# Optimization experiments

Hardware: AMD Instinct MI355X
Metric: run time of the kernel (lower is better)

The kernel has to match this reference:

```python
import jax, jax.numpy as jnp
import numpy as np
from jax import lax

EMBED_DIM = 384
NUM_GROUPS = 128
GROUP_SIZE = 64
LN_EPS = 1e-5


def setup_inputs() -> dict:
    key = jax.random.key(0)
    k_pts, k1, k2, k3, k4 = jax.random.split(key, 5)
    B, N = 32, 16384
    points = jax.random.normal(k_pts, (B, N, 3), dtype=jnp.float32)
    # local_mlp: Linear(3,128) -> GELU -> Linear(128, embed_dim)
    w1 = jax.random.normal(k1, (3, 128), dtype=jnp.float32) * (1.0 / np.sqrt(3))
    b1 = jax.random.normal(k2, (128,), dtype=jnp.float32) * 0.01
    w2 = jax.random.normal(k3, (128, EMBED_DIM), dtype=jnp.float32) * (1.0 / np.sqrt(128))
    b2 = jax.random.normal(k4, (EMBED_DIM,), dtype=jnp.float32) * 0.01
    ln_scale = jnp.ones((EMBED_DIM,), dtype=jnp.float32)
    ln_bias = jnp.zeros((EMBED_DIM,), dtype=jnp.float32)
    return {"points": points, "w1": w1, "b1": b1, "w2": w2, "b2": b2,
            "ln_scale": ln_scale, "ln_bias": ln_bias}


def _farthest_point_sample(points, num_samples):
    # points: [B, N, 3]. Deterministic start at index 0 (torch uses randint).
    B, N, _ = points.shape

    def step(carry, _):
        distance, farthest = carry  # [B, N], [B]
        centroid = jnp.take_along_axis(points, farthest[:, None, None], axis=1)  # [B,1,3]
        d = jnp.sum((points - centroid) ** 2, axis=-1)  # [B, N]
        distance = jnp.minimum(distance, d)
        nxt = jnp.argmax(distance, axis=-1).astype(jnp.int32)
        return (distance, nxt), farthest

    init = (jnp.full((B, N), jnp.inf, dtype=points.dtype),
            jnp.zeros((B,), dtype=jnp.int32))
    _, idx = lax.scan(step, init, None, length=num_samples)  # [S, B]
    return idx.T  # [B, S]


def reference(points, w1, b1, w2, b2, ln_scale, ln_bias):
    B, N, _ = points.shape
    centroid_idx = _farthest_point_sample(points, NUM_GROUPS)  # [B, G]
    centroids = jnp.take_along_axis(
        points, centroid_idx[:, :, None].astype(jnp.int32), axis=1)  # [B, G, 3]

    # squared distances (same ordering as torch.cdist for topk); matmul form
    # avoids materializing a [B, G, N, 3] diff tensor.
    c2 = jnp.sum(centroids ** 2, axis=-1)  # [B, G]
    p2 = jnp.sum(points ** 2, axis=-1)     # [B, N]
    dist2 = c2[:, :, None] + p2[:, None, :] - 2.0 * jnp.einsum(
        'bgc,bnc->bgn', centroids, points)  # [B, G, N]

    # k smallest -> top_k of negated distances
    _, neighbor_idx = lax.top_k(-dist2, GROUP_SIZE)  # [B, G, K]

    batch_ix = jnp.arange(B)[:, None, None]
    grouped = points[batch_ix, neighbor_idx]  # [B, G, K, 3]
    local_coords = grouped - centroids[:, :, None, :]  # [B, G, K, 3]

    h = jax.nn.gelu(local_coords @ w1 + b1, approximate=False)  # [B,G,K,128]
    feats = h @ w2 + b2  # [B, G, K, D]
    tokens = jnp.mean(feats, axis=2)  # [B, G, D]

    mu = jnp.mean(tokens, axis=-1, keepdims=True)
    var = jnp.mean((tokens - mu) ** 2, axis=-1, keepdims=True)
    tokens_ln = (tokens - mu) * lax.rsqrt(var + LN_EPS) * ln_scale + ln_bias
    return centroids, tokens_ln
```

## Files before the change

### kernel.cpp

```cpp
#include <hip/hip_runtime.h>
#include <math.h>

#define BB 32
#define NN 16384
#define GG 128
#define KK 64
#define HH 128
#define DD 384
#define LN_EPS 1e-5f
#define CAP 1024

__device__ __forceinline__ float sq3(float x, float y, float z) {
    return __fadd_rn(__fadd_rn(__fmul_rn(x, x), __fmul_rn(y, y)), __fmul_rn(z, z));
}

__device__ __forceinline__ unsigned distkey(float px, float py, float pz, float4 c4) {
    float p2 = sq3(px, py, pz);
    float dot = __fadd_rn(__fadd_rn(__fmul_rn(c4.x, px), __fmul_rn(c4.y, py)),
                          __fmul_rn(c4.z, pz));
    float d = __fsub_rn(__fadd_rn(c4.w, p2), __fmul_rn(2.0f, dot));
    unsigned u = __float_as_uint(d);
    return u ^ ((u & 0x80000000u) ? 0xFFFFFFFFu : 0x80000000u);
}

__device__ __forceinline__ unsigned lanerank(unsigned long long m) {
    unsigned r = __builtin_amdgcn_mbcnt_lo((unsigned)m, 0);
    return __builtin_amdgcn_mbcnt_hi((unsigned)(m >> 32), r);
}

__global__ void prep_kernel(const float* __restrict__ w2, float* __restrict__ w2t) {
    int i = blockIdx.x * 256 + threadIdx.x;
    if (i < HH * DD) {
        int f = i >> 7, k = i & 127;
        w2t[i] = w2[k * DD + f];
    }
}

__global__ __launch_bounds__(1024, 4) void fps_kernel(const float* __restrict__ pts,
                                                      float* __restrict__ cent_out,
                                                      float4* __restrict__ cent_pad) {
    __shared__ float4 ds4[NN / 4];
    __shared__ unsigned long long slot[GG];
    const int b = blockIdx.x;
    const int tid = threadIdx.x;
    const float* p = pts + (size_t)b * NN * 3;
    const float4* p4 = (const float4*)p;

    for (int i = tid; i < NN / 4; i += 1024)
        ds4[i] = make_float4(INFINITY, INFINITY, INFINITY, INFINITY);
    for (int i = tid; i < GG; i += 1024) slot[i] = 0ull;
    __syncthreads();

    float cx = p[0], cy = p[1], cz = p[2];

    for (int it = 0; it < GG; it++) {
        if (tid == 0) {
            float* co = cent_out + ((size_t)b * GG + it) * 3;
            co[0] = cx; co[1] = cy; co[2] = cz;
            cent_pad[b * GG + it] = make_float4(cx, cy, cz, sq3(cx, cy, cz));
        }
        if (it == GG - 1) break;

        float bv0 = -INFINITY, bv1 = -INFINITY, bv2 = -INFINITY, bv3 = -INFINITY;
        int bq0 = 0, bq1 = 0, bq2 = 0, bq3 = 0;
#pragma unroll
        for (int j = 0; j < 4; j++) {
            int q = tid + j * 1024;
            float4 A = p4[3 * q], B = p4[3 * q + 1], C = p4[3 * q + 2];
            float4 dv = ds4[q];
            float d0 = sq3(__fsub_rn(A.x, cx), __fsub_rn(A.y, cy), __fsub_rn(A.z, cz));
            float d1 = sq3(__fsub_rn(A.w, cx), __fsub_rn(B.x, cy), __fsub_rn(B.y, cz));
            float d2 = sq3(__fsub_rn(B.z, cx), __fsub_rn(B.w, cy), __fsub_rn(C.x, cz));
            float d3 = sq3(__fsub_rn(C.y, cx), __fsub_rn(C.z, cy), __fsub_rn(C.w, cz));
            float n0 = fminf(dv.x, d0), n1 = fminf(dv.y, d1);
            float n2 = fminf(dv.z, d2), n3 = fminf(dv.w, d3);
            bool ch = (d0 < dv.x) | (d1 < dv.y) | (d2 < dv.z) | (d3 < dv.w);
            if (ch) ds4[q] = make_float4(n0, n1, n2, n3);
            if (n0 > bv0) { bv0 = n0; bq0 = q; }
            if (n1 > bv1) { bv1 = n1; bq1 = q; }
            if (n2 > bv2) { bv2 = n2; bq2 = q; }
            if (n3 > bv3) { bv3 = n3; bq3 = q; }
        }
        float fv = bv0; int fi = 4 * bq0;
        {
            int i1 = 4 * bq1 + 1, i2 = 4 * bq2 + 2, i3 = 4 * bq3 + 3;
            if (bv1 > fv || (bv1 == fv && i1 < fi)) { fv = bv1; fi = i1; }
            if (bv2 > fv || (bv2 == fv && i2 < fi)) { fv = bv2; fi = i2; }
            if (bv3 > fv || (bv3 == fv && i3 < fi)) { fv = bv3; fi = i3; }
        }
#pragma unroll
        for (int off = 32; off >= 1; off >>= 1) {
            float ov = __shfl_down(fv, off);
            int oi = __shfl_down(fi, off);
            if (ov > fv || (ov == fv && oi < fi)) { fv = ov; fi = oi; }
        }
        if ((tid & 63) == 0) {
            unsigned long long packed =
                ((unsigned long long)__float_as_uint(fv) << 32) |
                (unsigned)(0xFFFFFFFFu - (unsigned)fi);
            atomicMax(&slot[it], packed);
        }
        __syncthreads();
        unsigned long long w = slot[it];
        int idx = (int)(0xFFFFFFFFu - (unsigned)w);
        const float* wp = p + (size_t)idx * 3;
        cx = wp[0]; cy = wp[1]; cz = wp[2];
    }
}

__global__ __launch_bounds__(256, 4) void group_kernel(
    const float* __restrict__ pts, const float4* __restrict__ cent_pad,
    const float* __restrict__ w1, const float* __restrict__ b1,
    const float* __restrict__ w2t, const float* __restrict__ b2,
    const float* __restrict__ lns, const float* __restrict__ lnb,
    float* __restrict__ tok_out) {
    __shared__ unsigned candKey[4][CAP];
    __shared__ unsigned short candIdx[4][CAP];
    __shared__ unsigned short tieIdx[4][128];
    __shared__ unsigned short selIdx[4][KK];
    __shared__ float4 localPt[4][KK];
    __shared__ __align__(16) float hbar[4][HH];

    const int tid = threadIdx.x, lane = tid & 63, wid = tid >> 6;
    const int x = blockIdx.x & 7, j = blockIdx.x >> 3;
    const int b = x * 4 + (j >> 5);
    const int g = ((j & 31) << 2) + wid;
    const float* p = pts + (size_t)b * NN * 3;
    const float4* p4 = (const float4*)p;
    float4 c4 = cent_pad[b * GG + g];

    unsigned sk[8];
#pragma unroll
    for (int s = 0; s < 8; s++) {
        int n = (s * 64 + lane) * 32;
        sk[s] = distkey(p[n * 3], p[n * 3 + 1], p[n * 3 + 2], c4);
    }
    auto sample_kth = [&](int rank) -> unsigned {
        unsigned T = 0u;
        for (int bit = 31; bit >= 0; bit--) {
            unsigned c = T | (1u << bit);
            int cnt = 0;
#pragma unroll
            for (int s = 0; s < 8; s++) cnt += __popcll(__ballot(sk[s] < c));
            if (cnt < rank) T = c;
        }
        return T;
    };
    unsigned* ck = candKey[wid];
    unsigned short* ci = candIdx[wid];

    unsigned T1 = sample_kth(16);
    int cnt;
    {
        int base = 0;
        for (int u = 0; u < 32; u++) {
            int qa = u * 128 + lane, qb = qa + 64;
            float4 Aa = p4[3 * qa], Ba = p4[3 * qa + 1], Ca = p4[3 * qa + 2];
            float4 Ab = p4[3 * qb], Bb2 = p4[3 * qb + 1], Cb = p4[3 * qb + 2];
#pragma unroll
            for (int t = 0; t < 2; t++) {
                int q = t ? qb : qa;
                float4 A = t ? Ab : Aa, Bv = t ? Bb2 : Ba, Cv = t ? Cb : Ca;
                unsigned kk[4];
                kk[0] = distkey(A.x, A.y, A.z, c4);
                kk[1] = distkey(A.w, Bv.x, Bv.y, c4);
                kk[2] = distkey(Bv.z, Bv.w, Cv.x, c4);
                kk[3] = distkey(Cv.y, Cv.z, Cv.w, c4);
#pragma unroll
                for (int qq = 0; qq < 4; qq++) {
                    bool pred = kk[qq] <= T1;
                    unsigned long long m = __ballot(pred);
                    if (pred) {
                        int pos = base + (int)lanerank(m);
                        if (pos < CAP) {
                            ck[pos] = kk[qq];
                            ci[pos] = (unsigned short)(4 * q + qq);
                        }
                    }
                    base += __popcll(m);
                }
            }
            if ((u & 3) == 3) __syncthreads();
        }
        cnt = base;
    }

    auto collect_ns = [&](unsigned T) -> int {
        int base = 0;
        for (int it2 = 0; it2 < 64; it2++) {
            int q = it2 * 64 + lane;
            float4 A = p4[3 * q], Bv = p4[3 * q + 1], Cv = p4[3 * q + 2];
            unsigned kk[4];
            kk[0] = distkey(A.x, A.y, A.z, c4);
            kk[1] = distkey(A.w, Bv.x, Bv.y, c4);
            kk[2] = distkey(Bv.z, Bv.w, Cv.x, c4);
            kk[3] = distkey(Cv.y, Cv.z, Cv.w, c4);
#pragma unroll
            for (int qq = 0; qq < 4; qq++) {
                bool pred = kk[qq] <= T;
                unsigned long long m = __ballot(pred);
                if (pred) {
                    int pos = base + (int)lanerank(m);
                    if (pos < CAP) {
                        ck[pos] = kk[qq];
                        ci[pos] = (unsigned short)(4 * q + qq);
                    }
                }
                base += __popcll(m);
            }
        }
        return base;
    };
    if (cnt > CAP) cnt = collect_ns(sample_kth(8));

    bool fallback = (cnt < KK || cnt > CAP);
    if (!fallback) {
        unsigned k8[16];
#pragma unroll
        for (int r = 0; r < 16; r++) {
            int s = r * 64 + lane;
            k8[r] = (s < cnt) ? ck[s] : 0xFFFFFFFFu;
        }
        unsigned T = 0u;
        for (int bit = 31; bit >= 0; bit--) {
            unsigned c = T | (1u << bit);
            int cl = 0;
#pragma unroll
            for (int r = 0; r < 16; r++) cl += __popcll(__ballot(k8[r] < c));
            if (cl < KK) T = c;
        }
        int cless = 0;
#pragma unroll
        for (int r = 0; r < 16; r++) cless += __popcll(__ballot(k8[r] < T));
        int need = KK - cless;
        int base2 = 0;
#pragma unroll
        for (int r = 0; r < 16; r++) {
            bool pr = k8[r] < T;
            unsigned long long m = __ballot(pr);
            if (pr) selIdx[wid][base2 + lanerank(m)] = ci[r * 64 + lane];
            base2 += __popcll(m);
        }
        int tb = 0;
#pragma unroll
        for (int r = 0; r < 16; r++) {
            bool pr = (r * 64 + lane < cnt) && (k8[r] == T);
            unsigned long long m = __ballot(pr);
            if (pr) {
                int pos = tb + (int)lanerank(m);
                if (pos < 128) tieIdx[wid][pos] = ci[r * 64 + lane];
            }
            tb += __popcll(m);
        }
        if (tb > 128) {
            fallback = true;
        } else {
#pragma unroll
            for (int rr = 0; rr < 2; rr++) {
                int t = lane + rr * 64;
                if (t < tb) {
                    unsigned short my = tieIdx[wid][t];
                    int rank = 0;
                    for (int j2 = 0; j2 < tb; j2++) rank += (tieIdx[wid][j2] < my);
                    if (rank < need) selIdx[wid][cless + rank] = my;
                }
            }
        }
    }
    if (fallback) {
        unsigned long long last = 0ull;
        for (int r = 0; r < KK; r++) {
            unsigned long long best = ~0ull;
            for (int it2 = 0; it2 < 64; it2++) {
                int q = it2 * 64 + lane;
                float4 A = p4[3 * q], Bv = p4[3 * q + 1], Cv = p4[3 * q + 2];
                unsigned kk[4];
                kk[0] = distkey(A.x, A.y, A.z, c4);
                kk[1] = distkey(A.w, Bv.x, Bv.y, c4);
                kk[2] = distkey(Bv.z, Bv.w, Cv.x, c4);
                kk[3] = distkey(Cv.y, Cv.z, Cv.w, c4);
#pragma unroll
                for (int qq = 0; qq < 4; qq++) {
                    unsigned long long pp =
                        (((unsigned long long)kk[qq]) << 16) | (unsigned)(4 * q + qq);
                    if ((r == 0 || pp > last) && pp < best) best = pp;
                }
            }
#pragma unroll
            for (int off = 32; off >= 1; off >>= 1) {
                unsigned long long o = __shfl_xor(best, off);
                if (o < best) best = o;
            }
            selIdx[wid][r] = (unsigned short)(best & 0xFFFFu);
            last = best;
        }
    }
    __syncthreads();

    {
        int n = selIdx[wid][lane];
        localPt[wid][lane] =
            make_float4(p[n * 3] - c4.x, p[n * 3 + 1] - c4.y, p[n * 3 + 2] - c4.z, 0.f);
    }
    {
        float wa0 = w1[lane], wb0 = w1[HH + lane], wc0 = w1[2 * HH + lane], bb0 = b1[lane];
        float wa1 = w1[64 + lane], wb1 = w1[HH + 64 + lane], wc1 = w1[2 * HH + 64 + lane],
              bb1 = b1[64 + lane];
        float s0 = 0.f, s1 = 0.f;
        for (int k = 0; k < KK; k++) {
            float4 lp = localPt[wid][k];
            float a0 = lp.x * wa0 + lp.y * wb0 + lp.z * wc0 + bb0;
            float a1 = lp.x * wa1 + lp.y * wb1 + lp.z * wc1 + bb1;
            s0 += 0.5f * a0 * (1.0f + erff(a0 * 0.70710678118654752440f));
            s1 += 0.5f * a1 * (1.0f + erff(a1 * 0.70710678118654752440f));
        }
        hbar[wid][lane] = s0 * (1.0f / 64.0f);
        hbar[wid][64 + lane] = s1 * (1.0f / 64.0f);
    }
    {
        const int f0 = lane * 6;
        float acc0 = b2[f0], acc1 = b2[f0 + 1], acc2 = b2[f0 + 2];
        float acc3 = b2[f0 + 3], acc4 = b2[f0 + 4], acc5 = b2[f0 + 5];
        const float4* hb = (const float4*)hbar[wid];
        for (int q = 0; q < HH / 4; q++) {
            float4 h4 = hb[q];
            const float* w0 = w2t + (size_t)f0 * HH + 4 * q;
            float4 a = *(const float4*)(w0);
            float4 bq = *(const float4*)(w0 + HH);
            float4 cq = *(const float4*)(w0 + 2 * HH);
            float4 dq = *(const float4*)(w0 + 3 * HH);
            float4 eq = *(const float4*)(w0 + 4 * HH);
            float4 fq = *(const float4*)(w0 + 5 * HH);
            acc0 += h4.x * a.x + h4.y * a.y + h4.z * a.z + h4.w * a.w;
            acc1 += h4.x * bq.x + h4.y * bq.y + h4.z * bq.z + h4.w * bq.w;
            acc2 += h4.x * cq.x + h4.y * cq.y + h4.z * cq.z + h4.w * cq.w;
            acc3 += h4.x * dq.x + h4.y * dq.y + h4.z * dq.z + h4.w * dq.w;
            acc4 += h4.x * eq.x + h4.y * eq.y + h4.z * eq.z + h4.w * eq.w;
            acc5 += h4.x * fq.x + h4.y * fq.y + h4.z * fq.z + h4.w * fq.w;
        }
        float s1v = acc0 + acc1 + acc2 + acc3 + acc4 + acc5;
        float s2v = acc0 * acc0 + acc1 * acc1 + acc2 * acc2 + acc3 * acc3 +
                    acc4 * acc4 + acc5 * acc5;
#pragma unroll
        for (int off = 32; off >= 1; off >>= 1) {
            s1v += __shfl_xor(s1v, off);
            s2v += __shfl_xor(s2v, off);
        }
        float mu = s1v / (float)DD;
        float var = s2v / (float)DD - mu * mu;
        float rstd = rsqrtf(var + LN_EPS);
        float* outp = tok_out + ((size_t)b * GG + g) * DD + f0;
        outp[0] = (acc0 - mu) * rstd * lns[f0] + lnb[f0];
        outp[1] = (acc1 - mu) * rstd * lns[f0 + 1] + lnb[f0 + 1];
        outp[2] = (acc2 - mu) * rstd * lns[f0 + 2] + lnb[f0 + 2];
        outp[3] = (acc3 - mu) * rstd * lns[f0 + 3] + lnb[f0 + 3];
        outp[4] = (acc4 - mu) * rstd * lns[f0 + 4] + lnb[f0 + 4];
        outp[5] = (acc5 - mu) * rstd * lns[f0 + 5] + lnb[f0 + 5];
    }
}

extern "C" void kernel_launch(void* const* d_in, const int* in_sizes, int n_in,
                              void* d_out, int out_size, void* d_ws, size_t ws_size,
                              hipStream_t stream) {
    const float* pts = (const float*)d_in[0];
    const float* w1 = (const float*)d_in[1];
    const float* b1 = (const float*)d_in[2];
    const float* w2 = (const float*)d_in[3];
    const float* b2 = (const float*)d_in[4];
    const float* lns = (const float*)d_in[5];
    const float* lnb = (const float*)d_in[6];
    float* out = (float*)d_out;

    float4* cent_pad = (float4*)d_ws;
    float* w2t = (float*)((char*)d_ws + 65536);

    prep_kernel<<<192, 256, 0, stream>>>(w2, w2t);
    fps_kernel<<<BB, 1024, 0, stream>>>(pts, out, cent_pad);
    group_kernel<<<1024, 256, 0, stream>>>(pts, cent_pad, w1, b1, w2t, b2, lns, lnb,
                                           out + BB * GG * 3);
}
```

Baseline: 591.3 us.

## Fuse FPS and grouping into one persistent kernel with per-centroid ready flags

Merges the farthest-point-sampling kernel and the grouping/MLP kernel into one persistent kernel. The first 32 blocks run FPS and publish each centroid index through a global flag. Every wave, including FPS waves once they finish, pulls (batch, group) tasks from an atomic counter and spins until that centroid is ready. The goal is to overlap kNN and MLP work with the serial FPS iterations instead of waiting for FPS to complete. The candidate capacity shrinks and the sampled threshold rank changes to cut shared memory, at the cost of spin-waiting, a smaller CU footprint for FPS blocks, and more reliance on the fallback path.

```diff
diff --git a/kernel.cpp b/kernel.cpp
--- a/kernel.cpp
+++ b/kernel.cpp
@@ -8,7 +8,8 @@
 #define HH 128
 #define DD 384
 #define LN_EPS 1e-5f
-#define CAP 1024
+#define CAP 640
+#define NTASK (BB * GG)
 
 __device__ __forceinline__ float sq3(float x, float y, float z) {
     return __fadd_rn(__fadd_rn(__fmul_rn(x, x), __fmul_rn(y, y)), __fmul_rn(z, z));
@@ -28,139 +29,159 @@
     return __builtin_amdgcn_mbcnt_hi((unsigned)(m >> 32), r);
 }
 
-__global__ void prep_kernel(const float* __restrict__ w2, float* __restrict__ w2t) {
+__global__ void prep_kernel(const float* __restrict__ w2, float* __restrict__ w2t,
+                            unsigned* __restrict__ syncArea) {
     int i = blockIdx.x * 256 + threadIdx.x;
     if (i < HH * DD) {
         int f = i >> 7, k = i & 127;
         w2t[i] = w2[k * DD + f];
     }
-}
-
-__global__ __launch_bounds__(1024, 4) void fps_kernel(const float* __restrict__ pts,
-                                                      float* __restrict__ cent_out,
-                                                      float4* __restrict__ cent_pad) {
-    __shared__ float4 ds4[NN / 4];
+    if (i < NTASK + 64) syncArea[i] = 0u;
+}
+
+struct GrpSh {
+    unsigned candKey[16][CAP];
+    unsigned short candIdx[16][CAP];
+    unsigned short tieIdx[16][128];
+    unsigned short selIdx[16][KK];
+    float4 localPt[16][KK];
+    float hbar[16][HH];
+};
+struct FpsSh {
+    float4 ds4[NN / 4];
+};
+union ShU {
+    FpsSh f;
+    GrpSh g;
+};
+
+__global__ __launch_bounds__(1024) void fused_kernel(
+    const float* __restrict__ pts, const float* __restrict__ w1,
+    const float* __restrict__ b1, const float* __restrict__ w2t,
+    const float* __restrict__ b2, const float* __restrict__ lns,
+    const float* __restrict__ lnb, float* __restrict__ cent_out,
+    float* __restrict__ tok_out, unsigned* __restrict__ done,
+    unsigned* __restrict__ taskCtr) {
+    __shared__ ShU sh;
     __shared__ unsigned long long slot[GG];
-    const int b = blockIdx.x;
-    const int tid = threadIdx.x;
-    const float* p = pts + (size_t)b * NN * 3;
-    const float4* p4 = (const float4*)p;
-
-    for (int i = tid; i < NN / 4; i += 1024)
-        ds4[i] = make_float4(INFINITY, INFINITY, INFINITY, INFINITY);
-    for (int i = tid; i < GG; i += 1024) slot[i] = 0ull;
+    const int tid = threadIdx.x, lane = tid & 63, wid = tid >> 6;
+
+    if (blockIdx.x < BB) {
+        const int b = blockIdx.x;
+        const float* p = pts + (size_t)b * NN * 3;
+        const float4* p4 = (const float4*)p;
+        for (int i = tid; i < NN / 4; i += 1024)
+            sh.f.ds4[i] = make_float4(INFINITY, INFINITY, INFINITY, INFINITY);
+        for (int i = tid; i < GG; i += 1024) slot[i] = 0ull;
+        __syncthreads();
+
+        float cx = p[0], cy = p[1], cz = p[2];
+        int curIdx = 0;
+        for (int it = 0; it < GG; it++) {
+            if (tid == 0) {
+                float* co = cent_out + ((size_t)b * GG + it) * 3;
+                co[0] = cx; co[1] = cy; co[2] = cz;
+                __hip_atomic_store(&done[b * GG + it], (unsigned)(curIdx + 1),
+                                   __ATOMIC_RELAXED, __HIP_MEMORY_SCOPE_AGENT);
+            }
+            if (it == GG - 1) break;
+
+            float bv0 = -INFINITY, bv1 = -INFINITY, bv2 = -INFINITY, bv3 = -INFINITY;
+            int bq0 = 0, bq1 = 0, bq2 = 0, bq3 = 0;
+#pragma unroll
+            for (int j = 0; j < 4; j++) {
+                int q = tid + j * 1024;
+                float4 A = p4[3 * q], B = p4[3 * q + 1], C = p4[3 * q + 2];
+                float4 dv = sh.f.ds4[q];
+                float d0 = sq3(__fsub_rn(A.x, cx), __fsub_rn(A.y, cy), __fsub_rn(A.z, cz));
+                float d1 = sq3(__fsub_rn(A.w, cx), __fsub_rn(B.x, cy), __fsub_rn(B.y, cz));
+                float d2 = sq3(__fsub_rn(B.z, cx), __fsub_rn(B.w, cy), __fsub_rn(C.x, cz));
+                float d3 = sq3(__fsub_rn(C.y, cx), __fsub_rn(C.z, cy), __fsub_rn(C.w, cz));
+                float n0 = fminf(dv.x, d0), n1 = fminf(dv.y, d1);
+                float n2 = fminf(dv.z, d2), n3 = fminf(dv.w, d3);
+                bool ch = (d0 < dv.x) | (d1 < dv.y) | (d2 < dv.z) | (d3 < dv.w);
+                if (ch) sh.f.ds4[q] = make_float4(n0, n1, n2, n3);
+                if (n0 > bv0) { bv0 = n0; bq0 = q; }
+                if (n1 > bv1) { bv1 = n1; bq1 = q; }
+                if (n2 > bv2) { bv2 = n2; bq2 = q; }
+                if (n3 > bv3) { bv3 = n3; bq3 = q; }
+            }
+            float fv = bv0; int fi = 4 * bq0;
+            {
+                int i1 = 4 * bq1 + 1, i2 = 4 * bq2 + 2, i3 = 4 * bq3 + 3;
+                if (bv1 > fv || (bv1 == fv && i1 < fi)) { fv = bv1; fi = i1; }
+                if (bv2 > fv || (bv2 == fv && i2 < fi)) { fv = bv2; fi = i2; }
+                if (bv3 > fv || (bv3 == fv && i3 < fi)) { fv = bv3; fi = i3; }
+            }
+#pragma unroll
+            for (int off = 32; off >= 1; off >>= 1) {
+                float ov = __shfl_down(fv, off);
+                int oi = __shfl_down(fi, off);
+                if (ov > fv || (ov == fv && oi < fi)) { fv = ov; fi = oi; }
+            }
+            if ((tid & 63) == 0) {
+                unsigned long long packed =
+                    ((unsigned long long)__float_as_uint(fv) << 32) |
+                    (unsigned)(0xFFFFFFFFu - (unsigned)fi);
+                atomicMax(&slot[it], packed);
+            }
+            __syncthreads();
+            unsigned long long w = slot[it];
+            curIdx = (int)(0xFFFFFFFFu - (unsigned)w);
+            const float* wp = p + (size_t)curIdx * 3;
+            cx = wp[0]; cy = wp[1]; cz = wp[2];
+        }
+    }
     __syncthreads();
 
-    float cx = p[0], cy = p[1], cz = p[2];
-
-    for (int it = 0; it < GG; it++) {
-        if (tid == 0) {
-            float* co = cent_out + ((size_t)b * GG + it) * 3;
-            co[0] = cx; co[1] = cy; co[2] = cz;
-            cent_pad[b * GG + it] = make_float4(cx, cy, cz, sq3(cx, cy, cz));
-        }
-        if (it == GG - 1) break;
-
-        float bv0 = -INFINITY, bv1 = -INFINITY, bv2 = -INFINITY, bv3 = -INFINITY;
-        int bq0 = 0, bq1 = 0, bq2 = 0, bq3 = 0;
-#pragma unroll
-        for (int j = 0; j < 4; j++) {
-            int q = tid + j * 1024;
-            float4 A = p4[3 * q], B = p4[3 * q + 1], C = p4[3 * q + 2];
-            float4 dv = ds4[q];
-            float d0 = sq3(__fsub_rn(A.x, cx), __fsub_rn(A.y, cy), __fsub_rn(A.z, cz));
-            float d1 = sq3(__fsub_rn(A.w, cx), __fsub_rn(B.x, cy), __fsub_rn(B.y, cz));
-            float d2 = sq3(__fsub_rn(B.z, cx), __fsub_rn(B.w, cy), __fsub_rn(C.x, cz));
-            float d3 = sq3(__fsub_rn(C.y, cx), __fsub_rn(C.z, cy), __fsub_rn(C.w, cz));
-            float n0 = fminf(dv.x, d0), n1 = fminf(dv.y, d1);
-            float n2 = fminf(dv.z, d2), n3 = fminf(dv.w, d3);
-            bool ch = (d0 < dv.x) | (d1 < dv.y) | (d2 < dv.z) | (d3 < dv.w);
-            if (ch) ds4[q] = make_float4(n0, n1, n2, n3);
-            if (n0 > bv0) { bv0 = n0; bq0 = q; }
-            if (n1 > bv1) { bv1 = n1; bq1 = q; }
-            if (n2 > bv2) { bv2 = n2; bq2 = q; }
-            if (n3 > bv3) { bv3 = n3; bq3 = q; }
-        }
-        float fv = bv0; int fi = 4 * bq0;
-        {
-            int i1 = 4 * bq1 + 1, i2 = 4 * bq2 + 2, i3 = 4 * bq3 + 3;
-            if (bv1 > fv || (bv1 == fv && i1 < fi)) { fv = bv1; fi = i1; }
-            if (bv2 > fv || (bv2 == fv && i2 < fi)) { fv = bv2; fi = i2; }
-            if (bv3 > fv || (bv3 == fv && i3 < fi)) { fv = bv3; fi = i3; }
-        }
-#pragma unroll
-        for (int off = 32; off >= 1; off >>= 1) {
-            float ov = __shfl_down(fv, off);
-            int oi = __shfl_down(fi, off);
-            if (ov > fv || (ov == fv && oi < fi)) { fv = ov; fi = oi; }
-        }
-        if ((tid & 63) == 0) {
-            unsigned long long packed =
-                ((unsigned long long)__float_as_uint(fv) << 32) |
-                (unsigned)(0xFFFFFFFFu - (unsigned)fi);
-            atomicMax(&slot[it], packed);
-        }
-        __syncthreads();
-        unsigned long long w = slot[it];
-        int idx = (int)(0xFFFFFFFFu - (unsigned)w);
-        const float* wp = p + (size_t)idx * 3;
-        cx = wp[0]; cy = wp[1]; cz = wp[2];
-    }
-}
-
-__global__ __launch_bounds__(256, 4) void group_kernel(
-    const float* __restrict__ pts, const float4* __restrict__ cent_pad,
-    const float* __restrict__ w1, const float* __restrict__ b1,
-    const float* __restrict__ w2t, const float* __restrict__ b2,
-    const float* __restrict__ lns, const float* __restrict__ lnb,
-    float* __restrict__ tok_out) {
-    __shared__ unsigned candKey[4][CAP];
-    __shared__ unsigned short candIdx[4][CAP];
-    __shared__ unsigned short tieIdx[4][128];
-    __shared__ unsigned short selIdx[4][KK];
-    __shared__ float4 localPt[4][KK];
-    __shared__ __align__(16) float hbar[4][HH];
-
-    const int tid = threadIdx.x, lane = tid & 63, wid = tid >> 6;
-    const int x = blockIdx.x & 7, j = blockIdx.x >> 3;
-    const int b = x * 4 + (j >> 5);
-    const int g = ((j & 31) << 2) + wid;
-    const float* p = pts + (size_t)b * NN * 3;
-    const float4* p4 = (const float4*)p;
-    float4 c4 = cent_pad[b * GG + g];
-
-    unsigned sk[8];
-#pragma unroll
-    for (int s = 0; s < 8; s++) {
-        int n = (s * 64 + lane) * 32;
-        sk[s] = distkey(p[n * 3], p[n * 3 + 1], p[n * 3 + 2], c4);
-    }
-    auto sample_kth = [&](int rank) -> unsigned {
-        unsigned T = 0u;
-        for (int bit = 31; bit >= 0; bit--) {
-            unsigned c = T | (1u << bit);
-            int cnt = 0;
-#pragma unroll
-            for (int s = 0; s < 8; s++) cnt += __popcll(__ballot(sk[s] < c));
-            if (cnt < rank) T = c;
-        }
-        return T;
-    };
-    unsigned* ck = candKey[wid];
-    unsigned short* ci = candIdx[wid];
-
-    unsigned T1 = sample_kth(16);
-    int cnt;
-    {
-        int base = 0;
-        for (int u = 0; u < 32; u++) {
-            int qa = u * 128 + lane, qb = qa + 64;
-            float4 Aa = p4[3 * qa], Ba = p4[3 * qa + 1], Ca = p4[3 * qa + 2];
-            float4 Ab = p4[3 * qb], Bb2 = p4[3 * qb + 1], Cb = p4[3 * qb + 2];
-#pragma unroll
-            for (int t = 0; t < 2; t++) {
-                int q = t ? qb : qa;
-                float4 A = t ? Ab : Aa, Bv = t ? Bb2 : Ba, Cv = t ? Cb : Ca;
+    for (;;) {
+        unsigned t;
+        if (lane == 0)
+            t = __hip_atomic_fetch_add(taskCtr, 1u, __ATOMIC_RELAXED,
+                                       __HIP_MEMORY_SCOPE_AGENT);
+        t = (unsigned)__shfl((int)t, 0);
+        if (t >= NTASK) break;
+        const int b = (int)(t & 31u);
+        const int g = (int)(t >> 5);
+
+        unsigned v;
+        do {
+            v = __hip_atomic_load(&done[b * GG + g], __ATOMIC_RELAXED,
+                                  __HIP_MEMORY_SCOPE_AGENT);
+            if (v) break;
+            __builtin_amdgcn_s_sleep(4);
+        } while (true);
+
+        const float* p = pts + (size_t)b * NN * 3;
+        const float4* p4 = (const float4*)p;
+        const int cidx = (int)v - 1;
+        float ccx = p[3 * cidx], ccy = p[3 * cidx + 1], ccz = p[3 * cidx + 2];
+        float4 c4 = make_float4(ccx, ccy, ccz, sq3(ccx, ccy, ccz));
+
+        unsigned sk[8];
+#pragma unroll
+        for (int s = 0; s < 8; s++) {
+            int n = (s * 64 + lane) * 32;
+            sk[s] = distkey(p[n * 3], p[n * 3 + 1], p[n * 3 + 2], c4);
+        }
+        auto sample_kth = [&](int rank) -> unsigned {
+            unsigned T = 0u;
+            for (int bit = 31; bit >= 0; bit--) {
+                unsigned c = T | (1u << bit);
+                int cnt2 = 0;
+#pragma unroll
+                for (int s = 0; s < 8; s++) cnt2 += __popcll(__ballot(sk[s] < c));
+                if (cnt2 < rank) T = c;
+            }
+            return T;
+        };
+        unsigned* ck = sh.g.candKey[wid];
+        unsigned short* ci = sh.g.candIdx[wid];
+        auto collect = [&](unsigned T) -> int {
+            int base = 0;
+            for (int it2 = 0; it2 < 64; it2++) {
+                int q = it2 * 64 + lane;
+                float4 A = p4[3 * q], Bv = p4[3 * q + 1], Cv = p4[3 * q + 2];
                 unsigned kk[4];
                 kk[0] = distkey(A.x, A.y, A.z, c4);
                 kk[1] = distkey(A.w, Bv.x, Bv.y, c4);
@@ -168,7 +189,7 @@
                 kk[3] = distkey(Cv.y, Cv.z, Cv.w, c4);
 #pragma unroll
                 for (int qq = 0; qq < 4; qq++) {
-                    bool pred = kk[qq] <= T1;
+                    bool pred = kk[qq] <= T;
                     unsigned long long m = __ballot(pred);
                     if (pred) {
                         int pos = base + (int)lanerank(m);
@@ -180,182 +201,157 @@
                     base += __popcll(m);
                 }
             }
-            if ((u & 3) == 3) __syncthreads();
-        }
-        cnt = base;
-    }
-
-    auto collect_ns = [&](unsigned T) -> int {
-        int base = 0;
-        for (int it2 = 0; it2 < 64; it2++) {
-            int q = it2 * 64 + lane;
-            float4 A = p4[3 * q], Bv = p4[3 * q + 1], Cv = p4[3 * q + 2];
-            unsigned kk[4];
-            kk[0] = distkey(A.x, A.y, A.z, c4);
-            kk[1] = distkey(A.w, Bv.x, Bv.y, c4);
-            kk[2] = distkey(Bv.z, Bv.w, Cv.x, c4);
-            kk[3] = distkey(Cv.y, Cv.z, Cv.w, c4);
-#pragma unroll
-            for (int qq = 0; qq < 4; qq++) {
-                bool pred = kk[qq] <= T;
-                unsigned long long m = __ballot(pred);
-                if (pred) {
-                    int pos = base + (int)lanerank(m);
-                    if (pos < CAP) {
-                        ck[pos] = kk[qq];
-                        ci[pos] = (unsigned short)(4 * q + qq);
+            return base;
+        };
+
+        int cnt = collect(sample_kth(8));
+        if (cnt > CAP) cnt = collect(sample_kth(4));
+
+        bool fallback = (cnt < KK || cnt > CAP);
+        if (!fallback) {
+            unsigned k8[10];
+#pragma unroll
+            for (int r = 0; r < 10; r++) {
+                int s = r * 64 + lane;
+                k8[r] = (s < cnt) ? ck[s] : 0xFFFFFFFFu;
+            }
+            unsigned T = 0u;
+            for (int bit = 31; bit >= 0; bit--) {
+                unsigned c = T | (1u << bit);
+                int cl = 0;
+#pragma unroll
+                for (int r = 0; r < 10; r++) cl += __popcll(__ballot(k8[r] < c));
+                if (cl < KK) T = c;
+            }
+            int cless = 0;
+#pragma unroll
+            for (int r = 0; r < 10; r++) cless += __popcll(__ballot(k8[r] < T));
+            int need = KK - cless;
+            int base2 = 0;
+#pragma unroll
+            for (int r = 0; r < 10; r++) {
+                bool pr = k8[r] < T;
+                unsigned long long m = __ballot(pr);
+                if (pr) sh.g.selIdx[wid][base2 + lanerank(m)] = ci[r * 64 + lane];
+                base2 += __popcll(m);
+            }
+            int tb = 0;
+#pragma unroll
+            for (int r = 0; r < 10; r++) {
+                bool pr = (r * 64 + lane < cnt) && (k8[r] == T);
+                unsigned long long m = __ballot(pr);
+                if (pr) {
+                    int pos = tb + (int)lanerank(m);
+                    if (pos < 128) sh.g.tieIdx[wid][pos] = ci[r * 64 + lane];
+                }
+                tb += __popcll(m);
+            }
+            if (tb > 128) {
+                fallback = true;
+            } else {
+#pragma unroll
+                for (int rr = 0; rr < 2; rr++) {
+                    int tt = lane + rr * 64;
+                    if (tt < tb) {
+                        unsigned short my = sh.g.tieIdx[wid][tt];
+                        int rank = 0;
+                        for (int j2 = 0; j2 < tb; j2++)
+                            rank += (sh.g.tieIdx[wid][j2] < my);
+                        if (rank < need) sh.g.selIdx[wid][cless + rank] = my;
                     }
                 }
-                base += __popcll(m);
-            }
-        }
-        return base;
-    };
-    if (cnt > CAP) cnt = collect_ns(sample_kth(8));
-
-    bool fallback = (cnt < KK || cnt > CAP);
-    if (!fallback) {
-        unsigned k8[16];
-#pragma unroll
-        for (int r = 0; r < 16; r++) {
-            int s = r * 64 + lane;
-            k8[r] = (s < cnt) ? ck[s] : 0xFFFFFFFFu;
-        }
-        unsigned T = 0u;
-        for (int bit = 31; bit >= 0; bit--) {
-            unsigned c = T | (1u << bit);
-            int cl = 0;
-#pragma unroll
-            for (int r = 0; r < 16; r++) cl += __popcll(__ballot(k8[r] < c));
-            if (cl < KK) T = c;
-        }
-        int cless = 0;
-#pragma unroll
-        for (int r = 0; r < 16; r++) cless += __popcll(__ballot(k8[r] < T));
-        int need = KK - cless;
-        int base2 = 0;
-#pragma unroll
-        for (int r = 0; r < 16; r++) {
-            bool pr = k8[r] < T;
-            unsigned long long m = __ballot(pr);
-            if (pr) selIdx[wid][base2 + lanerank(m)] = ci[r * 64 + lane];
-            base2 += __popcll(m);
-        }
-        int tb = 0;
-#pragma unroll
-        for (int r = 0; r < 16; r++) {
-            bool pr = (r * 64 + lane < cnt) && (k8[r] == T);
-            unsigned long long m = __ballot(pr);
-            if (pr) {
-                int pos = tb + (int)lanerank(m);
-                if (pos < 128) tieIdx[wid][pos] = ci[r * 64 + lane];
-            }
-            tb += __popcll(m);
-        }
-        if (tb > 128) {
-            fallback = true;
-        } else {
-#pragma unroll
-            for (int rr = 0; rr < 2; rr++) {
-                int t = lane + rr * 64;
-                if (t < tb) {
-                    unsigned short my = tieIdx[wid][t];
-                    int rank = 0;
-                    for (int j2 = 0; j2 < tb; j2++) rank += (tieIdx[wid][j2] < my);
-                    if (rank < need) selIdx[wid][cless + rank] = my;
-                }
-            }
-        }
-    }
-    if (fallback) {
-        unsigned long long last = 0ull;
-        for (int r = 0; r < KK; r++) {
-            unsigned long long best = ~0ull;
-            for (int it2 = 0; it2 < 64; it2++) {
-                int q = it2 * 64 + lane;
-                float4 A = p4[3 * q], Bv = p4[3 * q + 1], Cv = p4[3 * q + 2];
-                unsigned kk[4];
-                kk[0] = distkey(A.x, A.y, A.z, c4);
-                kk[1] = distkey(A.w, Bv.x, Bv.y, c4);
-                kk[2] = distkey(Bv.z, Bv.w, Cv.x, c4);
-                kk[3] = distkey(Cv.y, Cv.z, Cv.w, c4);
-#pragma unroll
-                for (int qq = 0; qq < 4; qq++) {
-                    unsigned long long pp =
-                        (((unsigned long long)kk[qq]) << 16) | (unsigned)(4 * q + qq);
-                    if ((r == 0 || pp > last) && pp < best) best = pp;
-                }
-            }
+            }
+        }
+        if (fallback) {
+            unsigned long long last = 0ull;
+            for (int r = 0; r < KK; r++) {
+                unsigned long long best = ~0ull;
+                for (int it2 = 0; it2 < 64; it2++) {
+                    int q = it2 * 64 + lane;
+                    float4 A = p4[3 * q], Bv = p4[3 * q + 1], Cv = p4[3 * q + 2];
+                    unsigned kk[4];
+                    kk[0] = distkey(A.x, A.y, A.z, c4);
+                    kk[1] = distkey(A.w, Bv.x, Bv.y, c4);
+                    kk[2] = distkey(Bv.z, Bv.w, Cv.x, c4);
+                    kk[3] = distkey(Cv.y, Cv.z, Cv.w, c4);
+#pragma unroll
+                    for (int qq = 0; qq < 4; qq++) {
+                        unsigned long long pp =
+                            (((unsigned long long)kk[qq]) << 16) | (unsigned)(4 * q + qq);
+                        if ((r == 0 || pp > last) && pp < best) best = pp;
+                    }
+                }
+#pragma unroll
+                for (int off = 32; off >= 1; off >>= 1) {
+                    unsigned long long o = __shfl_xor(best, off);
+                    if (o < best) best = o;
+                }
+                sh.g.selIdx[wid][r] = (unsigned short)(best & 0xFFFFu);
+                last = best;
+            }
+        }
+
+        {
+            int n = sh.g.selIdx[wid][lane];
+            sh.g.localPt[wid][lane] = make_float4(p[n * 3] - c4.x, p[n * 3 + 1] - c4.y,
+                                                  p[n * 3 + 2] - c4.z, 0.f);
+        }
+        {
+            float wa0 = w1[lane], wb0 = w1[HH + lane], wc0 = w1[2 * HH + lane],
+                  bb0 = b1[lane];
+            float wa1 = w1[64 + lane], wb1 = w1[HH + 64 + lane],
+                  wc1 = w1[2 * HH + 64 + lane], bb1 = b1[64 + lane];
+            float s0 = 0.f, s1 = 0.f;
+            for (int k = 0; k < KK; k++) {
+                float4 lp = sh.g.localPt[wid][k];
+                float a0 = lp.x * wa0 + lp.y * wb0 + lp.z * wc0 + bb0;
+                float a1 = lp.x * wa1 + lp.y * wb1 + lp.z * wc1 + bb1;
+                s0 += 0.5f * a0 * (1.0f + erff(a0 * 0.70710678118654752440f));
+                s1 += 0.5f * a1 * (1.0f + erff(a1 * 0.70710678118654752440f));
+            }
+            sh.g.hbar[wid][lane] = s0 * (1.0f / 64.0f);
+            sh.g.hbar[wid][64 + lane] = s1 * (1.0f / 64.0f);
+        }
+        {
+            const int f0 = lane * 6;
+            float acc0 = b2[f0], acc1 = b2[f0 + 1], acc2 = b2[f0 + 2];
+            float acc3 = b2[f0 + 3], acc4 = b2[f0 + 4], acc5 = b2[f0 + 5];
+            const float4* hb = (const float4*)sh.g.hbar[wid];
+            for (int q = 0; q < HH / 4; q++) {
+                float4 h4 = hb[q];
+                const float* w0 = w2t + (size_t)f0 * HH + 4 * q;
+                float4 a = *(const float4*)(w0);
+                float4 bq = *(const float4*)(w0 + HH);
+                float4 cq = *(const float4*)(w0 + 2 * HH);
+                float4 dq = *(const float4*)(w0 + 3 * HH);
+                float4 eq = *(const float4*)(w0 + 4 * HH);
+                float4 fq = *(const float4*)(w0 + 5 * HH);
+                acc0 += h4.x * a.x + h4.y * a.y + h4.z * a.z + h4.w * a.w;
+                acc1 += h4.x * bq.x + h4.y * bq.y + h4.z * bq.z + h4.w * bq.w;
+                acc2 += h4.x * cq.x + h4.y * cq.y + h4.z * cq.z + h4.w * cq.w;
+                acc3 += h4.x * dq.x + h4.y * dq.y + h4.z * dq.z + h4.w * dq.w;
+                acc4 += h4.x * eq.x + h4.y * eq.y + h4.z * eq.z + h4.w * eq.w;
+                acc5 += h4.x * fq.x + h4.y * fq.y + h4.z * fq.z + h4.w * fq.w;
+            }
+            float s1v = acc0 + acc1 + acc2 + acc3 + acc4 + acc5;
+            float s2v = acc0 * acc0 + acc1 * acc1 + acc2 * acc2 + acc3 * acc3 +
+                        acc4 * acc4 + acc5 * acc5;
 #pragma unroll
             for (int off = 32; off >= 1; off >>= 1) {
-                unsigned long long o = __shfl_xor(best, off);
-                if (o < best) best = o;
-            }
-            selIdx[wid][r] = (unsigned short)(best & 0xFFFFu);
-            last = best;
-        }
-    }
-    __syncthreads();
-
-    {
-        int n = selIdx[wid][lane];
-        localPt[wid][lane] =
-            make_float4(p[n * 3] - c4.x, p[n * 3 + 1] - c4.y, p[n * 3 + 2] - c4.z, 0.f);
-    }
-    {
-        float wa0 = w1[lane], wb0 = w1[HH + lane], wc0 = w1[2 * HH + lane], bb0 = b1[lane];
-        float wa1 = w1[64 + lane], wb1 = w1[HH + 64 + lane], wc1 = w1[2 * HH + 64 + lane],
-              bb1 = b1[64 + lane];
-        float s0 = 0.f, s1 = 0.f;
-        for (int k = 0; k < KK; k++) {
-            float4 lp = localPt[wid][k];
-            float a0 = lp.x * wa0 + lp.y * wb0 + lp.z * wc0 + bb0;
-            float a1 = lp.x * wa1 + lp.y * wb1 + lp.z * wc1 + bb1;
-            s0 += 0.5f * a0 * (1.0f + erff(a0 * 0.70710678118654752440f));
-            s1 += 0.5f * a1 * (1.0f + erff(a1 * 0.70710678118654752440f));
-        }
-        hbar[wid][lane] = s0 * (1.0f / 64.0f);
-        hbar[wid][64 + lane] = s1 * (1.0f / 64.0f);
-    }
-    {
-        const int f0 = lane * 6;
-        float acc0 = b2[f0], acc1 = b2[f0 + 1], acc2 = b2[f0 + 2];
-        float acc3 = b2[f0 + 3], acc4 = b2[f0 + 4], acc5 = b2[f0 + 5];
-        const float4* hb = (const float4*)hbar[wid];
-        for (int q = 0; q < HH / 4; q++) {
-            float4 h4 = hb[q];
-            const float* w0 = w2t + (size_t)f0 * HH + 4 * q;
-            float4 a = *(const float4*)(w0);
-            float4 bq = *(const float4*)(w0 + HH);
-            float4 cq = *(const float4*)(w0 + 2 * HH);
-            float4 dq = *(const float4*)(w0 + 3 * HH);
-            float4 eq = *(const float4*)(w0 + 4 * HH);
-            float4 fq = *(const float4*)(w0 + 5 * HH);
-            acc0 += h4.x * a.x + h4.y * a.y + h4.z * a.z + h4.w * a.w;
-            acc1 += h4.x * bq.x + h4.y * bq.y + h4.z * bq.z + h4.w * bq.w;
-            acc2 += h4.x * cq.x + h4.y * cq.y + h4.z * cq.z + h4.w * cq.w;
-            acc3 += h4.x * dq.x + h4.y * dq.y + h4.z * dq.z + h4.w * dq.w;
-            acc4 += h4.x * eq.x + h4.y * eq.y + h4.z * eq.z + h4.w * eq.w;
-            acc5 += h4.x * fq.x + h4.y * fq.y + h4.z * fq.z + h4.w * fq.w;
-        }
-        float s1v = acc0 + acc1 + acc2 + acc3 + acc4 + acc5;
-        float s2v = acc0 * acc0 + acc1 * acc1 + acc2 * acc2 + acc3 * acc3 +
-                    acc4 * acc4 + acc5 * acc5;
-#pragma unroll
-        for (int off = 32; off >= 1; off >>= 1) {
-            s1v += __shfl_xor(s1v, off);
-            s2v += __shfl_xor(s2v, off);
-        }
-        float mu = s1v / (float)DD;
-        float var = s2v / (float)DD - mu * mu;
-        float rstd = rsqrtf(var + LN_EPS);
-        float* outp = tok_out + ((size_t)b * GG + g) * DD + f0;
-        outp[0] = (acc0 - mu) * rstd * lns[f0] + lnb[f0];
-        outp[1] = (acc1 - mu) * rstd * lns[f0 + 1] + lnb[f0 + 1];
-        outp[2] = (acc2 - mu) * rstd * lns[f0 + 2] + lnb[f0 + 2];
-        outp[3] = (acc3 - mu) * rstd * lns[f0 + 3] + lnb[f0 + 3];
-        outp[4] = (acc4 - mu) * rstd * lns[f0 + 4] + lnb[f0 + 4];
-        outp[5] = (acc5 - mu) * rstd * lns[f0 + 5] + lnb[f0 + 5];
+                s1v += __shfl_xor(s1v, off);
+                s2v += __shfl_xor(s2v, off);
+            }
+            float mu = s1v / (float)DD;
+            float var = s2v / (float)DD - mu * mu;
+            float rstd = rsqrtf(var + LN_EPS);
+            float* outp = tok_out + ((size_t)b * GG + g) * DD + f0;
+            outp[0] = (acc0 - mu) * rstd * lns[f0] + lnb[f0];
+            outp[1] = (acc1 - mu) * rstd * lns[f0 + 1] + lnb[f0 + 1];
+            outp[2] = (acc2 - mu) * rstd * lns[f0 + 2] + lnb[f0 + 2];
+            outp[3] = (acc3 - mu) * rstd * lns[f0 + 3] + lnb[f0 + 3];
+            outp[4] = (acc4 - mu) * rstd * lns[f0 + 4] + lnb[f0 + 4];
+            outp[5] = (acc5 - mu) * rstd * lns[f0 + 5] + lnb[f0 + 5];
+        }
     }
 }
 
@@ -371,11 +367,12 @@
     const float* lnb = (const float*)d_in[6];
     float* out = (float*)d_out;
 
-    float4* cent_pad = (float4*)d_ws;
-    float* w2t = (float*)((char*)d_ws + 65536);
-
-    prep_kernel<<<192, 256, 0, stream>>>(w2, w2t);
-    fps_kernel<<<BB, 1024, 0, stream>>>(pts, out, cent_pad);
-    group_kernel<<<1024, 256, 0, stream>>>(pts, cent_pad, w1, b1, w2t, b2, lns, lnb,
-                                           out + BB * GG * 3);
-}
+    float* w2t = (float*)d_ws;
+    unsigned* syncArea = (unsigned*)((char*)d_ws + 196608);
+    unsigned* done = syncArea;
+    unsigned* taskCtr = syncArea + NTASK;
+
+    prep_kernel<<<192, 256, 0, stream>>>(w2, w2t, syncArea);
+    fused_kernel<<<256, 1024, 0, stream>>>(pts, w1, b1, w2t, b2, lns, lnb,
+                                           out, out + BB * GG * 3, done, taskCtr);
+}
```

After: 1.770 ms. +199.3%, slower.
